# Optimization experiments

Hardware: AMD Instinct MI355X
Metric: run time of the kernel (lower is better)

Reference implementation:

```python
import jax, jax.numpy as jnp
import numpy as np

B, S, D, H, HD = 2, 2048, 1024, 16, 64


def setup_inputs() -> dict:
    key = jax.random.key(0)
    ks = jax.random.split(key, 5)
    sc = 1.0 / np.sqrt(D)  # lecun-normal-ish scale for kernels
    return {
        "x": jax.random.normal(ks[0], (B, S, D), jnp.float32),
        "Wq": jax.random.normal(ks[1], (D, H, HD), jnp.float32) * sc,
        "bq": jnp.zeros((H, HD), jnp.float32),
        "Wk": jax.random.normal(ks[2], (D, H, HD), jnp.float32) * sc,
        "bk": jnp.zeros((H, HD), jnp.float32),
        "Wv": jax.random.normal(ks[3], (D, H, HD), jnp.float32) * sc,
        "bv": jnp.zeros((H, HD), jnp.float32),
        "Wo": jax.random.normal(ks[4], (H, HD, D), jnp.float32) * (1.0 / np.sqrt(H * HD)),
        "bo": jnp.zeros((D,), jnp.float32),
    }


def reference(x, Wq, bq, Wk, bk, Wv, bv, Wo, bo):
    # QKV projections: [B,S,D] x [D,H,Hd] -> [B,S,H,Hd]
    q = jnp.einsum("bsd,dhk->bshk", x, Wq) + bq
    k = jnp.einsum("bsd,dhk->bshk", x, Wk) + bk
    v = jnp.einsum("bsd,dhk->bshk", x, Wv) + bv
    depth = q.shape[-1]
    q = q / jnp.sqrt(jnp.asarray(depth, q.dtype))
    # attention weights [B,H,Sq,Sk]
    attn = jnp.einsum("bqhd,bkhd->bhqk", q, k)
    attn = jax.nn.softmax(attn, axis=-1)
    # weighted values [B,Sq,H,Hd]
    out = jnp.einsum("bhqk,bkhd->bqhd", attn, v)
    # output projection back to d_model
    return jnp.einsum("bqhd,hdm->bqm", out, Wo) + bo
```

## Files before the change

### kernel.cpp

```cpp
#include <hip/hip_runtime.h>


typedef __attribute__((ext_vector_type(8))) short short8;
typedef __attribute__((ext_vector_type(4))) float float4v;

__device__ __forceinline__ void async16(void* lds, const void* g) {
  __builtin_amdgcn_global_load_lds(
      (__attribute__((address_space(1))) void*)(g),
      (__attribute__((address_space(3))) void*)(lds), 16, 0, 0);
}

__device__ __forceinline__ short f2bf(float f) {
  union { float f; unsigned u; } v;
  v.f = f;
  unsigned r = v.u + 0x7fffu + ((v.u >> 16) & 1u);
  return (short)(r >> 16);
}

#if __has_builtin(__builtin_amdgcn_cvt_pk_bf16_f32)
__device__ __forceinline__ unsigned pk2(float a, float b) {
  auto h = __builtin_amdgcn_cvt_pk_bf16_f32(a, b);
  unsigned u;
  __builtin_memcpy(&u, &h, 4);
  return u;
}
#else
__device__ __forceinline__ unsigned pk2(float a, float b) {
  return (unsigned)(unsigned short)f2bf(a) |
         ((unsigned)(unsigned short)f2bf(b) << 16);
}
#endif

#if __has_builtin(__builtin_amdgcn_exp2f)
__device__ __forceinline__ float fexp2(float x) { return __builtin_amdgcn_exp2f(x); }
#else
__device__ __forceinline__ float fexp2(float x) { return exp2f(x); }
#endif

__device__ __forceinline__ short8 cvt8(const float* __restrict__ g) {
  float4v a = *(const float4v*)(g);
  float4v b = *(const float4v*)(g + 4);
  union { unsigned u[4]; short8 s; } r;
  r.u[0] = pk2(a[0], a[1]);
  r.u[1] = pk2(a[2], a[3]);
  r.u[2] = pk2(b[0], b[1]);
  r.u[3] = pk2(b[2], b[3]);
  return r.s;
}

__device__ __forceinline__ void mfma_tile(const short* As, const short* Bs,
                                          float4v acc[4][4]) {
  int t = threadIdx.x, lane = t & 63, w = t >> 6, r = lane & 15, q = lane >> 4;
  int wr = (w >> 1) * 64, wc = (w & 1) * 64;
  short8 af[4], bfr[4];
#pragma unroll
  for (int mt = 0; mt < 4; mt++)
    af[mt] = *(const short8*)(As + (wr + mt * 16 + r) * 32 + q * 8);
#pragma unroll
  for (int nt = 0; nt < 4; nt++)
    bfr[nt] = *(const short8*)(Bs + (wc + nt * 16 + r) * 32 + q * 8);
#pragma unroll
  for (int mt = 0; mt < 4; mt++)
#pragma unroll
    for (int nt = 0; nt < 4; nt++)
      acc[mt][nt] = __builtin_amdgcn_mfma_f32_16x16x32_bf16(
          af[mt], bfr[nt], acc[mt][nt], 0, 0, 0);
}

__global__ __launch_bounds__(256) void convw_t3(
    const float* __restrict__ W0, const float* __restrict__ W1,
    const float* __restrict__ W2, short* __restrict__ dst) {
  __shared__ short tile[64][65];
  int z = blockIdx.z;
  const float* src = (z == 0) ? W0 : (z == 1) ? W1 : W2;
  short* d = dst + z * 1048576;
  int r0 = blockIdx.y * 64, c0 = blockIdx.x * 64;
  int t = threadIdx.x;
#pragma unroll
  for (int i = 0; i < 16; i++) {
    int e = i * 256 + t;
    int r = e >> 6, c = e & 63;
    tile[r][c] = f2bf(src[(r0 + r) * 1024 + c0 + c]);
  }
  __syncthreads();
#pragma unroll
  for (int i = 0; i < 16; i++) {
    int e = i * 256 + t;
    int r = e >> 6, c = e & 63;
    d[(c0 + r) * 1024 + r0 + c] = tile[c][r];
  }
}

__global__ __launch_bounds__(256) void convwo_t(
    const float* __restrict__ W, short* __restrict__ d) {
  __shared__ short tile[64][65];
  int r0 = blockIdx.y * 64, c0 = blockIdx.x * 64;
  int t = threadIdx.x;
#pragma unroll
  for (int i = 0; i < 16; i++) {
    int e = i * 256 + t;
    int r = e >> 6, c = e & 63;
    tile[r][c] = f2bf(W[(r0 + r) * 1024 + c0 + c]);
  }
  __syncthreads();
#pragma unroll
  for (int i = 0; i < 16; i++) {
    int e = i * 256 + t;
    int r = e >> 6, c = e & 63;
    d[(c0 + r) * 1024 + r0 + c] = tile[c][r];
  }
}

__global__ __launch_bounds__(256) void conv_x(
    const float* __restrict__ x, short* __restrict__ xb) {
  int i = (blockIdx.x * 256 + threadIdx.x) * 8;
  *(short8*)(xb + i) = cvt8(x + i);
}

__global__ __launch_bounds__(256, 2) void qkv_gemm_fast(
    const short* __restrict__ xb, const short* __restrict__ WT,
    const float* __restrict__ bq, const float* __restrict__ bk,
    const float* __restrict__ bv, short* __restrict__ Qd,
    short* __restrict__ Kd, short* __restrict__ Vt0, short* __restrict__ Vt1) {
  __shared__ __align__(16) short As[4096];
  __shared__ __align__(16) short Bs[4096];
  int z = blockIdx.z;
  int t = threadIdx.x;
  int m0, n0;
  if (z < 2) { m0 = blockIdx.y * 128; n0 = blockIdx.x * 128; }
  else       { m0 = blockIdx.x * 128; n0 = blockIdx.y * 128; }
  const short* Wz = WT + z * 1048576;
  const short* A = (z < 2) ? xb : Wz;
  const short* B = (z < 2) ? Wz : xb;
  float4v acc[4][4];
#pragma unroll
  for (int mt = 0; mt < 4; mt++)
#pragma unroll
    for (int nt = 0; nt < 4; nt++)
#pragma unroll
      for (int k = 0; k < 4; k++) acc[mt][nt][k] = 0.0f;

  for (int kt = 0; kt < 32; kt++) {
    int k0 = kt * 32;
    __syncthreads();
#pragma unroll
    for (int i = 0; i < 2; i++) {
      int p = i * 256 + t;
      int rr = p >> 2, cc = p & 3;
      async16(As + p * 8, A + (m0 + rr) * 1024 + k0 + cc * 8);
      async16(Bs + p * 8, B + (n0 + rr) * 1024 + k0 + cc * 8);
    }
    __syncthreads();
    mfma_tile(As, Bs, acc);
  }
  int lane = t & 63, w = t >> 6, r = lane & 15, q = lane >> 4;
  int wr = (w >> 1) * 64, wc = (w & 1) * 64;
  if (z < 2) {
    const float* bias = (z == 0) ? bq : bk;
    short* dst = (z == 0) ? Qd : Kd;
    float scale = (z == 0) ? 0.1803368801111204f : 1.0f;
#pragma unroll
    for (int mt = 0; mt < 4; mt++)
#pragma unroll
      for (int reg = 0; reg < 4; reg++) {
        int m = m0 + wr + mt * 16 + q * 4 + reg;
        int b = m >> 11, s = m & 2047;
#pragma unroll
        for (int nt = 0; nt < 4; nt++) {
          int n = n0 + wc + nt * 16 + r;
          int h = n >> 6, hd = n & 63;
          float v = (acc[mt][nt][reg] + bias[n]) * scale;
          dst[((b * 16 + h) << 17) + (s << 6) + hd] = f2bf(v);
        }
      }
  } else {
#pragma unroll
    for (int mt = 0; mt < 4; mt++)
#pragma unroll
      for (int reg = 0; reg < 4; reg++) {
        int mrow = m0 + wr + mt * 16 + q * 4 + reg;
        int h = mrow >> 6, hd = mrow & 63;
        float bias = bv[mrow];
#pragma unroll
        for (int nt = 0; nt < 4; nt++) {
          int n = n0 + wc + nt * 16 + r;
          int b = n >> 11, s = n & 2047;
          int idx = b * 16 + h;
          short* vp = (idx < 16) ? (Vt0 + idx * 131072)
                                 : (Vt1 + (idx - 16) * 131072);
          vp[(hd << 11) + s] = f2bf(acc[mt][nt][reg] + bias);
        }
      }
  }
}

__global__ __launch_bounds__(256, 4) void attn_kernel(
    short* __restrict__ QO, const short* __restrict__ K,
    const short* __restrict__ V0, const short* __restrict__ V1) {
  __shared__ __align__(16) short Qs[64 * 64];
  __shared__ __align__(16) short Ks[64 * 64];
  __shared__ __align__(16) short Vs[64 * 64];
  __shared__ __align__(16) short Ps[4 * 16 * 72];
  int qt = blockIdx.x, bh = blockIdx.y;
  int t = threadIdx.x, lane = t & 63, w = t >> 6, r = lane & 15, q = lane >> 4;
  int r7 = r & 7;
  short* Qb = QO + bh * 131072 + qt * 4096;
  const short* Kb = K + bh * 131072;
  const short* Vb = (bh < 16) ? (V0 + bh * 131072) : (V1 + (bh - 16) * 131072);
#pragma unroll
  for (int i = 0; i < 2; i++) {
    int p = i * 256 + t;
    int rr = p >> 3, c = p & 7;
    async16(Qs + p * 8, Qb + rr * 64 + (c ^ (rr & 7)) * 8);
  }
  __syncthreads();
  short8 aq[2];
#pragma unroll
  for (int ks = 0; ks < 2; ks++) {
    int ph = ((ks * 4 + q) ^ r7) * 8;
    aq[ks] = *(const short8*)(Qs + (w * 16 + r) * 64 + ph);
  }
  float4v accO[4];
  float lsum[4];
#pragma unroll
  for (int ht = 0; ht < 4; ht++)
#pragma unroll
    for (int k = 0; k < 4; k++) accO[ht][k] = 0.0f;
#pragma unroll
  for (int reg = 0; reg < 4; reg++) lsum[reg] = 0.0f;
  short* Pw = Ps + w * 16 * 72;

  for (int kt = 0; kt < 32; kt++) {
    __syncthreads();
#pragma unroll
    for (int i = 0; i < 2; i++) {
      int p = i * 256 + t;
      int rr = p >> 3, c = p & 7, cs = (c ^ (rr & 7)) * 8;
      async16(Ks + p * 8, Kb + kt * 4096 + rr * 64 + cs);
      async16(Vs + p * 8, Vb + kt * 64 + rr * 2048 + cs);
    }
    __syncthreads();
    float4v sc[4];
#pragma unroll
    for (int nt = 0; nt < 4; nt++)
#pragma unroll
      for (int k = 0; k < 4; k++) sc[nt][k] = 0.0f;
#pragma unroll
    for (int ks = 0; ks < 2; ks++) {
      int ph = ((ks * 4 + q) ^ r7) * 8;
      short8 bk8[4];
#pragma unroll
      for (int nt = 0; nt < 4; nt++)
        bk8[nt] = *(const short8*)(Ks + (nt * 16 + r) * 64 + ph);
#pragma unroll
      for (int nt = 0; nt < 4; nt++)
        sc[nt] = __builtin_amdgcn_mfma_f32_16x16x32_bf16(
            aq[ks], bk8[nt], sc[nt], 0, 0, 0);
    }
#pragma unroll
    for (int reg = 0; reg < 4; reg++) {
      float p0 = fexp2(sc[0][reg]);
      float p1 = fexp2(sc[1][reg]);
      float p2 = fexp2(sc[2][reg]);
      float p3 = fexp2(sc[3][reg]);
      lsum[reg] += (p0 + p1) + (p2 + p3);
      unsigned ua = pk2(p0, p1);
      unsigned ub = pk2(p2, p3);
      int base = (q * 4 + reg) * 72;
      Pw[base + 0 + r]  = (short)ua;
      Pw[base + 16 + r] = (short)(ua >> 16);
      Pw[base + 32 + r] = (short)ub;
      Pw[base + 48 + r] = (short)(ub >> 16);
    }
    __builtin_amdgcn_s_waitcnt(0xC07F);
#pragma unroll
    for (int ks = 0; ks < 2; ks++) {
      int ph = ((ks * 4 + q) ^ r7) * 8;
      short8 pa = *(const short8*)(Pw + r * 72 + ks * 32 + q * 8);
      short8 vb8[4];
#pragma unroll
      for (int ht = 0; ht < 4; ht++)
        vb8[ht] = *(const short8*)(Vs + (ht * 16 + r) * 64 + ph);
#pragma unroll
      for (int ht = 0; ht < 4; ht++)
        accO[ht] = __builtin_amdgcn_mfma_f32_16x16x32_bf16(
            pa, vb8[ht], accO[ht], 0, 0, 0);
    }
  }
#pragma unroll
  for (int reg = 0; reg < 4; reg++) {
    float l = lsum[reg];
#pragma unroll
    for (int d = 1; d < 16; d <<= 1) l += __shfl_xor(l, d);
    float inv = 1.0f / fmaxf(l, 1.0e-30f);
    int sl = w * 16 + q * 4 + reg;
#pragma unroll
    for (int ht = 0; ht < 4; ht++)
      Qb[sl * 64 + ht * 16 + r] = f2bf(accO[ht][reg] * inv);
  }
}

__global__ __launch_bounds__(256, 2) void out_gemm(
    const short* __restrict__ O, const short* __restrict__ WoT,
    const float* __restrict__ bo, float* __restrict__ out) {
  __shared__ __align__(16) short As[4096];
  __shared__ __align__(16) short Bs[2048];
  int m0 = blockIdx.y * 128, n0 = blockIdx.x * 64;
  int t = threadIdx.x, lane = t & 63, w = t >> 6, r = lane & 15, q = lane >> 4;
  int wr = (w >> 1) * 64, wc = (w & 1) * 32;
  float4v acc[4][2];
#pragma unroll
  for (int mt = 0; mt < 4; mt++)
#pragma unroll
    for (int nt = 0; nt < 2; nt++)
#pragma unroll
      for (int k = 0; k < 4; k++) acc[mt][nt][k] = 0.0f;

  for (int kt = 0; kt < 32; kt++) {
    int k0 = kt * 32;
    int h0 = k0 >> 6, hd0 = k0 & 63;
    __syncthreads();
#pragma unroll
    for (int i = 0; i < 2; i++) {
      int p = i * 256 + t;
      int rr = p >> 2, cc = p & 3;
      int m = m0 + rr;
      async16(As + p * 8, O + (m >> 11) * 2097152 + h0 * 131072 +
                              (m & 2047) * 64 + hd0 + cc * 8);
    }
    {
      int rr = t >> 2, cc = t & 3;
      async16(Bs + t * 8, WoT + (n0 + rr) * 1024 + k0 + cc * 8);
    }
    __syncthreads();
    short8 af[4], bfr[2];
#pragma unroll
    for (int mt = 0; mt < 4; mt++)
      af[mt] = *(const short8*)(As + (wr + mt * 16 + r) * 32 + q * 8);
#pragma unroll
    for (int nt = 0; nt < 2; nt++)
      bfr[nt] = *(const short8*)(Bs + (wc + nt * 16 + r) * 32 + q * 8);
#pragma unroll
    for (int mt = 0; mt < 4; mt++)
#pragma unroll
      for (int nt = 0; nt < 2; nt++)
        acc[mt][nt] = __builtin_amdgcn_mfma_f32_16x16x32_bf16(
            af[mt], bfr[nt], acc[mt][nt], 0, 0, 0);
  }
#pragma unroll
  for (int mt = 0; mt < 4; mt++)
#pragma unroll
    for (int reg = 0; reg < 4; reg++) {
      int m = m0 + wr + mt * 16 + q * 4 + reg;
#pragma unroll
      for (int nt = 0; nt < 2; nt++) {
        int n = n0 + wc + nt * 16 + r;
        out[m * 1024 + n] = acc[mt][nt][reg] + bo[n];
      }
    }
}

extern "C" void kernel_launch(void* const* d_in, const int* in_sizes, int n_in,
                              void* d_out, int out_size, void* d_ws,
                              size_t ws_size, hipStream_t stream) {
  (void)in_sizes; (void)n_in; (void)out_size; (void)ws_size;
  const float* x = (const float*)d_in[0];
  const float* Wq = (const float*)d_in[1];
  const float* bq = (const float*)d_in[2];
  const float* Wk = (const float*)d_in[3];
  const float* bk = (const float*)d_in[4];
  const float* Wv = (const float*)d_in[5];
  const float* bv = (const float*)d_in[6];
  const float* Wo = (const float*)d_in[7];
  const float* bo = (const float*)d_in[8];
  float* out = (float*)d_out;
  char* ws = (char*)d_ws;
  short* QO  = (short*)(ws);
  short* Kws = (short*)(ws + (8u << 20));
  short* WoT = (short*)(ws + (8u << 20));
  short* xb  = (short*)d_out;
  short* WT  = (short*)d_out + 4 * 1048576;
  short* Vt0 = (short*)Wq;
  short* Vt1 = (short*)Wk;

  dim3 tb(256);
  convw_t3<<<dim3(16, 16, 3), tb, 0, stream>>>(Wq, Wk, Wv, WT);
  conv_x<<<dim3(2048), tb, 0, stream>>>(x, xb);
  qkv_gemm_fast<<<dim3(8, 32, 3), tb, 0, stream>>>(xb, WT, bq, bk, bv,
                                                   QO, Kws, Vt0, Vt1);
  attn_kernel<<<dim3(32, 32), tb, 0, stream>>>(QO, Kws, Vt0, Vt1);
  convwo_t<<<dim3(16, 16), tb, 0, stream>>>(Wo, WoT);
  out_gemm<<<dim3(16, 32), tb, 0, stream>>>(QO, WoT, bo, out);
}
```

Measured before the change: 209.8 us.

## Restructure attention kernel with 32x32 MFMA, register-resident P and double-buffered KV

Rewrites the attention kernel to use 128-thread blocks, each wave owning 64 query rows. Scores are computed with 32x32x16 MFMAs as S^T, so the exp'd probabilities can be turned into the A operand of the PV MFMA through permlane32 swaps, with no LDS round-trip for P. K/V tiles are double-buffered so the next tile's async loads overlap compute, removing one barrier per iteration. The grid is flattened and remapped to 512 blocks. The trade-off is fewer blocks and waves with higher register pressure under launch_bounds(128,1), which may reduce occupancy and latency hiding.

```diff
diff --git a/kernel.cpp b/kernel.cpp
--- a/kernel.cpp
+++ b/kernel.cpp
@@ -3,6 +3,8 @@
 
 typedef __attribute__((ext_vector_type(8))) short short8;
 typedef __attribute__((ext_vector_type(4))) float float4v;
+typedef __attribute__((ext_vector_type(16))) float f32x16;
+typedef __attribute__((ext_vector_type(2))) int int2v;
 
 __device__ __forceinline__ void async16(void* lds, const void* g) {
   __builtin_amdgcn_global_load_lds(
@@ -36,6 +38,27 @@
 #else
 __device__ __forceinline__ float fexp2(float x) { return exp2f(x); }
 #endif
+
+__device__ __forceinline__ void plswap(unsigned& a, unsigned& b) {
+#if __has_builtin(__builtin_amdgcn_permlane32_swap)
+  int2v r = __builtin_amdgcn_permlane32_swap((int)a, (int)b, false, false);
+  a = (unsigned)r[0];
+  b = (unsigned)r[1];
+#else
+  unsigned ax = (unsigned)__shfl_xor((int)a, 32);
+  unsigned bx = (unsigned)__shfl_xor((int)b, 32);
+  bool hh = (threadIdx.x & 32) != 0;
+  a = hh ? bx : a;
+  b = hh ? b : ax;
+#endif
+}
+
+__device__ __forceinline__ short8 mk8(unsigned a, unsigned b, unsigned c,
+                                      unsigned d) {
+  union { unsigned u[4]; short8 s; } r;
+  r.u[0] = a; r.u[1] = b; r.u[2] = c; r.u[3] = d;
+  return r.s;
+}
 
 __device__ __forceinline__ short8 cvt8(const float* __restrict__ g) {
   float4v a = *(const float4v*)(g);
@@ -194,110 +217,138 @@
   }
 }
 
-__global__ __launch_bounds__(256, 4) void attn_kernel(
+__device__ __forceinline__ void stage_kv(short* Ksb, short* Vsb,
+                                         const short* Kt, const short* Vt,
+                                         int t) {
+#pragma unroll
+  for (int i = 0; i < 4; i++) {
+    int p = i * 128 + t, rr = p >> 3, c = p & 7, cs = (c ^ (rr & 7)) * 8;
+    async16(Ksb + p * 8, Kt + rr * 64 + cs);
+    async16(Vsb + p * 8, Vt + rr * 2048 + cs);
+  }
+}
+
+__global__ __launch_bounds__(128, 1) void attn_kernel(
     short* __restrict__ QO, const short* __restrict__ K,
     const short* __restrict__ V0, const short* __restrict__ V1) {
-  __shared__ __align__(16) short Qs[64 * 64];
-  __shared__ __align__(16) short Ks[64 * 64];
-  __shared__ __align__(16) short Vs[64 * 64];
-  __shared__ __align__(16) short Ps[4 * 16 * 72];
-  int qt = blockIdx.x, bh = blockIdx.y;
-  int t = threadIdx.x, lane = t & 63, w = t >> 6, r = lane & 15, q = lane >> 4;
-  int r7 = r & 7;
-  short* Qb = QO + bh * 131072 + qt * 4096;
+  __shared__ __align__(16) short Ks[2][4096];
+  __shared__ __align__(16) short Vs[2][4096];
+  __shared__ float sums[2][64];
+  int id = blockIdx.x;
+  int chunk = id >> 3;
+  int bh = (id & 7) * 4 + (chunk >> 4);
+  int qt = chunk & 15;
+  int t = threadIdx.x, lane = t & 63, w = t >> 6;
+  int l31 = lane & 31, hi = lane >> 5;
+  short* Qb = QO + bh * 131072;
   const short* Kb = K + bh * 131072;
   const short* Vb = (bh < 16) ? (V0 + bh * 131072) : (V1 + (bh - 16) * 131072);
-#pragma unroll
-  for (int i = 0; i < 2; i++) {
-    int p = i * 256 + t;
-    int rr = p >> 3, c = p & 7;
-    async16(Qs + p * 8, Qb + rr * 64 + (c ^ (rr & 7)) * 8);
-  }
+  int q0w = qt * 128 + w * 64;
+
+  short8 qf[2][4];
+#pragma unroll
+  for (int qb = 0; qb < 2; qb++)
+#pragma unroll
+    for (int ds = 0; ds < 4; ds++)
+      qf[qb][ds] =
+          *(const short8*)(Qb + (q0w + qb * 32 + l31) * 64 + ds * 16 + hi * 8);
+
+  f32x16 oacc[2][2];
+#pragma unroll
+  for (int qb = 0; qb < 2; qb++)
+#pragma unroll
+    for (int ht = 0; ht < 2; ht++)
+#pragma unroll
+      for (int i = 0; i < 16; i++) oacc[qb][ht][i] = 0.0f;
+  float lsum[2] = {0.0f, 0.0f};
+
+  stage_kv(Ks[0], Vs[0], Kb, Vb, t);
   __syncthreads();
-  short8 aq[2];
-#pragma unroll
-  for (int ks = 0; ks < 2; ks++) {
-    int ph = ((ks * 4 + q) ^ r7) * 8;
-    aq[ks] = *(const short8*)(Qs + (w * 16 + r) * 64 + ph);
-  }
-  float4v accO[4];
-  float lsum[4];
-#pragma unroll
-  for (int ht = 0; ht < 4; ht++)
-#pragma unroll
-    for (int k = 0; k < 4; k++) accO[ht][k] = 0.0f;
-#pragma unroll
-  for (int reg = 0; reg < 4; reg++) lsum[reg] = 0.0f;
-  short* Pw = Ps + w * 16 * 72;
 
   for (int kt = 0; kt < 32; kt++) {
+    int cur = kt & 1;
+    if (kt < 31)
+      stage_kv(Ks[cur ^ 1], Vs[cur ^ 1], Kb + (kt + 1) * 4096,
+               Vb + (kt + 1) * 64, t);
+    const short* Kc = Ks[cur];
+    const short* Vc = Vs[cur];
+#pragma unroll
+    for (int ck = 0; ck < 2; ck++) {
+      int kr = ck * 32 + l31;
+      short8 ka[4];
+#pragma unroll
+      for (int ds = 0; ds < 4; ds++)
+        ka[ds] =
+            *(const short8*)(Kc + kr * 64 + (((ds * 2 + hi) ^ (kr & 7)) * 8));
+      f32x16 sacc[2];
+#pragma unroll
+      for (int qb = 0; qb < 2; qb++)
+#pragma unroll
+        for (int i = 0; i < 16; i++) sacc[qb][i] = 0.0f;
+#pragma unroll
+      for (int ds = 0; ds < 4; ds++)
+#pragma unroll
+        for (int qb = 0; qb < 2; qb++)
+          sacc[qb] = __builtin_amdgcn_mfma_f32_32x32x16_bf16(
+              ka[ds], qf[qb][ds], sacc[qb], 0, 0, 0);
+      short8 pa[2][2];
+#pragma unroll
+      for (int qb = 0; qb < 2; qb++) {
+        float pv[16];
+#pragma unroll
+        for (int i = 0; i < 16; i++) pv[i] = fexp2(sacc[qb][i]);
+        lsum[qb] += (((pv[0] + pv[1]) + (pv[2] + pv[3])) +
+                     ((pv[4] + pv[5]) + (pv[6] + pv[7]))) +
+                    (((pv[8] + pv[9]) + (pv[10] + pv[11])) +
+                     ((pv[12] + pv[13]) + (pv[14] + pv[15])));
+        unsigned u0 = pk2(pv[0], pv[1]), u1 = pk2(pv[2], pv[3]);
+        unsigned u2 = pk2(pv[4], pv[5]), u3 = pk2(pv[6], pv[7]);
+        unsigned u4 = pk2(pv[8], pv[9]), u5 = pk2(pv[10], pv[11]);
+        unsigned u6 = pk2(pv[12], pv[13]), u7 = pk2(pv[14], pv[15]);
+        plswap(u0, u2);
+        plswap(u1, u3);
+        plswap(u4, u6);
+        plswap(u5, u7);
+        pa[qb][0] = mk8(u0, u1, u2, u3);
+        pa[qb][1] = mk8(u4, u5, u6, u7);
+      }
+#pragma unroll
+      for (int ks = 0; ks < 2; ks++) {
+        short8 vb8[2];
+#pragma unroll
+        for (int ht = 0; ht < 2; ht++) {
+          int d = ht * 32 + l31;
+          vb8[ht] = *(const short8*)(Vc + d * 64 +
+                                     (((ck * 4 + ks * 2 + hi) ^ (d & 7)) * 8));
+        }
+#pragma unroll
+        for (int qb = 0; qb < 2; qb++)
+#pragma unroll
+          for (int ht = 0; ht < 2; ht++)
+            oacc[qb][ht] = __builtin_amdgcn_mfma_f32_32x32x16_bf16(
+                pa[qb][ks], vb8[ht], oacc[qb][ht], 0, 0, 0);
+      }
+    }
     __syncthreads();
-#pragma unroll
-    for (int i = 0; i < 2; i++) {
-      int p = i * 256 + t;
-      int rr = p >> 3, c = p & 7, cs = (c ^ (rr & 7)) * 8;
-      async16(Ks + p * 8, Kb + kt * 4096 + rr * 64 + cs);
-      async16(Vs + p * 8, Vb + kt * 64 + rr * 2048 + cs);
-    }
-    __syncthreads();
-    float4v sc[4];
-#pragma unroll
-    for (int nt = 0; nt < 4; nt++)
-#pragma unroll
-      for (int k = 0; k < 4; k++) sc[nt][k] = 0.0f;
-#pragma unroll
-    for (int ks = 0; ks < 2; ks++) {
-      int ph = ((ks * 4 + q) ^ r7) * 8;
-      short8 bk8[4];
-#pragma unroll
-      for (int nt = 0; nt < 4; nt++)
-        bk8[nt] = *(const short8*)(Ks + (nt * 16 + r) * 64 + ph);
-#pragma unroll
-      for (int nt = 0; nt < 4; nt++)
-        sc[nt] = __builtin_amdgcn_mfma_f32_16x16x32_bf16(
-            aq[ks], bk8[nt], sc[nt], 0, 0, 0);
-    }
-#pragma unroll
-    for (int reg = 0; reg < 4; reg++) {
-      float p0 = fexp2(sc[0][reg]);
-      float p1 = fexp2(sc[1][reg]);
-      float p2 = fexp2(sc[2][reg]);
-      float p3 = fexp2(sc[3][reg]);
-      lsum[reg] += (p0 + p1) + (p2 + p3);
-      unsigned ua = pk2(p0, p1);
-      unsigned ub = pk2(p2, p3);
-      int base = (q * 4 + reg) * 72;
-      Pw[base + 0 + r]  = (short)ua;
-      Pw[base + 16 + r] = (short)(ua >> 16);
-      Pw[base + 32 + r] = (short)ub;
-      Pw[base + 48 + r] = (short)(ub >> 16);
-    }
-    __builtin_amdgcn_s_waitcnt(0xC07F);
-#pragma unroll
-    for (int ks = 0; ks < 2; ks++) {
-      int ph = ((ks * 4 + q) ^ r7) * 8;
-      short8 pa = *(const short8*)(Pw + r * 72 + ks * 32 + q * 8);
-      short8 vb8[4];
-#pragma unroll
-      for (int ht = 0; ht < 4; ht++)
-        vb8[ht] = *(const short8*)(Vs + (ht * 16 + r) * 64 + ph);
-#pragma unroll
-      for (int ht = 0; ht < 4; ht++)
-        accO[ht] = __builtin_amdgcn_mfma_f32_16x16x32_bf16(
-            pa, vb8[ht], accO[ht], 0, 0, 0);
-    }
-  }
-#pragma unroll
-  for (int reg = 0; reg < 4; reg++) {
-    float l = lsum[reg];
-#pragma unroll
-    for (int d = 1; d < 16; d <<= 1) l += __shfl_xor(l, d);
-    float inv = 1.0f / fmaxf(l, 1.0e-30f);
-    int sl = w * 16 + q * 4 + reg;
-#pragma unroll
-    for (int ht = 0; ht < 4; ht++)
-      Qb[sl * 64 + ht * 16 + r] = f2bf(accO[ht][reg] * inv);
-  }
+  }
+
+#pragma unroll
+  for (int qb = 0; qb < 2; qb++) {
+    float lt = lsum[qb] + __shfl_xor(lsum[qb], 32);
+    float inv = 1.0f / fmaxf(lt, 1.0e-30f);
+    if (lane < 32) sums[w][qb * 32 + l31] = inv;
+  }
+  __builtin_amdgcn_s_waitcnt(0xC07F);
+#pragma unroll
+  for (int qb = 0; qb < 2; qb++)
+#pragma unroll
+    for (int rg = 0; rg < 16; rg++) {
+      int srow = (rg & 3) + 8 * (rg >> 2) + 4 * hi;
+      float inv = sums[w][qb * 32 + srow];
+      short* orow = Qb + (q0w + qb * 32 + srow) * 64;
+      orow[l31] = f2bf(oacc[qb][0][rg] * inv);
+      orow[32 + l31] = f2bf(oacc[qb][1][rg] * inv);
+    }
 }
 
 __global__ __launch_bounds__(256, 2) void out_gemm(
@@ -388,7 +439,7 @@
   conv_x<<<dim3(2048), tb, 0, stream>>>(x, xb);
   qkv_gemm_fast<<<dim3(8, 32, 3), tb, 0, stream>>>(xb, WT, bq, bk, bv,
                                                    QO, Kws, Vt0, Vt1);
-  attn_kernel<<<dim3(32, 32), tb, 0, stream>>>(QO, Kws, Vt0, Vt1);
+  attn_kernel<<<dim3(512), dim3(128), 0, stream>>>(QO, Kws, Vt0, Vt1);
   convwo_t<<<dim3(16, 16), tb, 0, stream>>>(Wo, WoT);
   out_gemm<<<dim3(16, 32), tb, 0, stream>>>(QO, WoT, bo, out);
 }
```

Measured after the change: 243.2 us. 1.16x slower.
